# Performance work log

Hardware: AMD Instinct MI355X
Metric: run time of the kernel (lower is better)

## Reference

```python
import jax, jax.numpy as jnp
import numpy as np

B = 1024   # env batch (rollout step, T=1)
F = 512    # feature_size ('big' conv tower)
H = 128    # LSTM hidden size


def _conv(x, W, b, stride):
    # x: [B,Cin,H,W], W: [Cout,Cin,kh,kw]  (PyTorch NCHW / OIHW, VALID padding)
    y = jax.lax.conv_general_dilated(x, W, (stride, stride), 'VALID',
                                     dimension_numbers=('NCHW', 'OIHW', 'NCHW'))
    return y + b[None, :, None, None]


def _tower(x, W1, b1, W2, b2, W3, b3, Wl, bl):
    y = jax.nn.relu(_conv(x, W1, b1, 4))   # [B,32,20,20]
    y = jax.nn.relu(_conv(y, W2, b2, 2))   # [B,64,9,9]
    y = jax.nn.relu(_conv(y, W3, b3, 1))   # [B,64,7,7]
    y = y.reshape(y.shape[0], -1)          # [B,3136]
    return jax.nn.relu(y @ Wl.T + bl)      # [B,512]


def _ln(x, g, b):
    m = jnp.mean(x, -1, keepdims=True)
    v = jnp.var(x, -1, keepdims=True)
    return (x - m) * jax.lax.rsqrt(v + 1e-5) * g + b


def setup_inputs() -> dict:
    key = jax.random.key(0)
    ks = iter(jax.random.split(key, 64))
    rn = lambda shape, s=0.05: jax.random.normal(next(ks), shape, jnp.float32) * s
    inp = {
        'x': jax.random.normal(next(ks), (B, 2, 84, 84), jnp.float32),
        'done': (jax.random.uniform(next(ks), (B,)) < 0.1).astype(jnp.float32),
        'h0': rn((1, B, H), 0.1),
        'c0': rn((1, B, H), 0.1),
        # video tower
        'vW1': rn((32, 1, 8, 8)), 'vb1': jnp.zeros((32,), jnp.float32),
        'vW2': rn((64, 32, 4, 4)), 'vb2': jnp.zeros((64,), jnp.float32),
        'vW3': rn((64, 64, 3, 3)), 'vb3': jnp.zeros((64,), jnp.float32),
        'vWl': rn((F, 64 * 7 * 7)), 'vbl': jnp.zeros((F,), jnp.float32),
        # audio tower
        'aW1': rn((32, 1, 8, 8)), 'ab1': jnp.zeros((32,), jnp.float32),
        'aW2': rn((64, 32, 4, 4)), 'ab2': jnp.zeros((64,), jnp.float32),
        'aW3': rn((64, 64, 3, 3)), 'ab3': jnp.zeros((64,), jnp.float32),
        'aWl': rn((F, 64 * 7 * 7)), 'abl': jnp.zeros((F,), jnp.float32),
        # LayerNorms
        'vln_g': jnp.ones((F,), jnp.float32), 'vln_b': jnp.zeros((F,), jnp.float32),
        'aln_g': jnp.ones((F,), jnp.float32), 'aln_b': jnp.zeros((F,), jnp.float32),
        # CASL attention
        'att_vW': rn((32, F)), 'att_vb': jnp.zeros((32,), jnp.float32),
        'att_aW': rn((32, F)), 'att_ab': jnp.zeros((32,), jnp.float32),
        'att_sW': rn((32, H)), 'att_sb': jnp.zeros((32,), jnp.float32),
        'attW': rn((2, 32)), 'attb': jnp.zeros((2,), jnp.float32),
        # LSTM (PyTorch gate order i,f,g,o)
        'Wih': rn((4 * H, F)), 'Whh': rn((4 * H, H)),
        'bih': jnp.zeros((4 * H,), jnp.float32), 'bhh': jnp.zeros((4 * H,), jnp.float32),
    }
    return inp


def reference(x, done, h0, c0,
              vW1, vb1, vW2, vb2, vW3, vb3, vWl, vbl,
              aW1, ab1, aW2, ab2, aW3, ab3, aWl, abl,
              vln_g, vln_b, aln_g, aln_b,
              att_vW, att_vb, att_aW, att_ab, att_sW, att_sb, attW, attb,
              Wih, Whh, bih, bhh):
    # get_states with T=1 rollout step (batch_size = B)
    vf = _ln(_tower(x[:, 0:1], vW1, vb1, vW2, vb2, vW3, vb3, vWl, vbl), vln_g, vln_b)  # [B,512]
    af = _ln(_tower(x[:, 1:2], aW1, ab1, aW2, ab2, aW3, ab3, aWl, abl), aln_g, aln_b)  # [B,512]
    # attention gating
    act = jnp.tanh(vf @ att_vW.T + att_vb + af @ att_aW.T + att_ab
                   + h0[0] @ att_sW.T + att_sb)                    # [B,32]
    w = jax.nn.softmax(act @ attW.T + attb, axis=-1)               # [B,2]
    fused = w[:, 0:1] * vf + w[:, 1:2] * af                        # [B,512]
    # done-masked LSTM cell (single timestep)
    m = (1.0 - done)[:, None]
    h = m * h0[0]
    c = m * c0[0]
    gates = fused @ Wih.T + bih + h @ Whh.T + bhh                  # [B,512]
    i, f, g, o = jnp.split(gates, 4, axis=-1)
    c_new = jax.nn.sigmoid(f) * c + jax.nn.sigmoid(i) * jnp.tanh(g)
    h_new = jax.nn.sigmoid(o) * jnp.tanh(c_new)                    # [B,128]
    return h_new, c_new, vf, af
```

## Files before the change

kernel.cpp:

```cpp
#include <hip/hip_runtime.h>


typedef unsigned short u16;
typedef unsigned int u32;
typedef __attribute__((ext_vector_type(8))) short bf16x8;
typedef __attribute__((ext_vector_type(4))) float f32x4;

__device__ __forceinline__ float b2f(u16 u) {
    union { u32 i; float f; } v; v.i = ((u32)u) << 16; return v.f;
}
__device__ __forceinline__ u16 f2b(float f) {
    union { float f; u32 i; } v; v.f = f;
    u32 r = v.i + 0x7fffu + ((v.i >> 16) & 1u);
    return (u16)(r >> 16);
}
__device__ __forceinline__ void wave_lds_sync() {
    __builtin_amdgcn_wave_barrier();
    __builtin_amdgcn_s_waitcnt(0xC07F);
    __builtin_amdgcn_wave_barrier();
}

__global__ __launch_bounds__(256) void conv1_mfma(
    const float* __restrict__ x, long boff,
    const u16* __restrict__ Wp,
    const float* __restrict__ bias_v, const float* __restrict__ bias_a,
    u16* __restrict__ outp, int Mtot)
{
    __shared__ __attribute__((aligned(16))) u16 As[4 * 2304];

    const int tid = threadIdx.x;
    const int wave = tid >> 6, lane = tid & 63, quad = lane >> 4, l16 = lane & 15;
    const int t = blockIdx.y;
    const u16* Wpt = Wp + t * 2048;
    const float* bias = t ? bias_a : bias_v;
    u16* outt = outp + (long)t * Mtot * 32;

    const int mbase = blockIdx.x * 128 + wave * 32;
    const int rl = lane >> 1, h = lane & 1;
    int m = mbase + rl; if (m > Mtot - 1) m = Mtot - 1;
    const int bl = m / 400, p = m % 400;
    const int oy = p / 20, ox = p % 20;
    const float* F = x + boff + (long)bl * 14112 + t * 7056
                     + (long)(oy * 4) * 84 + ox * 4;

    {
        u16 tmp[32];
#pragma unroll
        for (int rr = 0; rr < 4; ++rr) {
            const int ky = h * 4 + rr;
            float4 v0 = *(const float4*)(F + ky * 84);
            float4 v1 = *(const float4*)(F + ky * 84 + 4);
            tmp[rr * 8 + 0] = f2b(v0.x); tmp[rr * 8 + 1] = f2b(v0.y);
            tmp[rr * 8 + 2] = f2b(v0.z); tmp[rr * 8 + 3] = f2b(v0.w);
            tmp[rr * 8 + 4] = f2b(v1.x); tmp[rr * 8 + 5] = f2b(v1.y);
            tmp[rr * 8 + 6] = f2b(v1.z); tmp[rr * 8 + 7] = f2b(v1.w);
        }
        u16* dst = As + wave * 2304 + rl * 72 + h * 32;
        const uint4* s = (const uint4*)tmp;
        *(uint4*)(dst)      = s[0];
        *(uint4*)(dst + 8)  = s[1];
        *(uint4*)(dst + 16) = s[2];
        *(uint4*)(dst + 24) = s[3];
    }
    wave_lds_sync();

    const u16* rb = As + wave * 2304;
    f32x4 acc[2][2];
#pragma unroll
    for (int mi = 0; mi < 2; ++mi)
#pragma unroll
        for (int ni = 0; ni < 2; ++ni)
            acc[mi][ni] = (f32x4){0.f, 0.f, 0.f, 0.f};

#pragma unroll
    for (int ks = 0; ks < 2; ++ks) {
        bf16x8 af[2], bf[2];
#pragma unroll
        for (int mi = 0; mi < 2; ++mi)
            af[mi] = *(const bf16x8*)(rb + (mi * 16 + l16) * 72 + ks * 32 + quad * 8);
#pragma unroll
        for (int ni = 0; ni < 2; ++ni)
            bf[ni] = *(const bf16x8*)(Wpt + ((ks * 2 + ni) * 64 + lane) * 8);
#pragma unroll
        for (int mi = 0; mi < 2; ++mi)
#pragma unroll
            for (int ni = 0; ni < 2; ++ni)
                acc[mi][ni] = __builtin_amdgcn_mfma_f32_16x16x32_bf16(
                    af[mi], bf[ni], acc[mi][ni], 0, 0, 0);
    }

#pragma unroll
    for (int mi = 0; mi < 2; ++mi)
#pragma unroll
        for (int ni = 0; ni < 2; ++ni) {
            const int col = ni * 16 + l16;
            const float bv = bias[col];
#pragma unroll
            for (int rr = 0; rr < 4; ++rr) {
                const int row = mbase + mi * 16 + quad * 4 + rr;
                if (row < Mtot)
                    outt[(long)row * 32 + col] = f2b(fmaxf(acc[mi][ni][rr] + bv, 0.f));
            }
        }
}

template<int IC, int IH, int IW, int OC, int KH, int KW, int S, int OH, int OW>
__global__ __launch_bounds__(256) void convW_mfma(
    const u16* __restrict__ in, long inTs,
    const u16* __restrict__ Wp, int WpTs,
    const float* __restrict__ bias_v, const float* __restrict__ bias_a,
    u16* __restrict__ outp, long outTs, int Mtot)
{
    constexpr int OP  = OH * OW;
    constexpr int K   = KH * KW * IC;
    constexpr int NF  = OC / 16;
    constexpr int NCH = K / 64;

    __shared__ __attribute__((aligned(16))) u16 As[4 * 2 * 2304];

    const int tid = threadIdx.x;
    const int wave = tid >> 6, lane = tid & 63, quad = lane >> 4, l16 = lane & 15;
    const int t = blockIdx.y;
    const u16* int_ = in + (long)t * inTs;
    const u16* Wpt = Wp + (long)t * WpTs;
    const float* bias = t ? bias_a : bias_v;
    u16* outt = outp + (long)t * outTs;

    const int mbase = blockIdx.x * 128 + wave * 32;
    const int rl = lane >> 1, h = lane & 1;
    int m = mbase + rl; if (m > Mtot - 1) m = Mtot - 1;
    const int bl = m / OP, p = m % OP;
    const int oy = p / OW, ox = p % OW;
    const u16* abase = int_ + (((long)bl * IH + oy * S) * IW + ox * S) * IC + h * 32;

    u16* wbase = As + wave * 4608 + rl * 72 + h * 32;
    const u16* rbase = As + wave * 4608;

    f32x4 acc[2][NF];
#pragma unroll
    for (int mi = 0; mi < 2; ++mi)
#pragma unroll
        for (int ni = 0; ni < NF; ++ni)
            acc[mi][ni] = (f32x4){0.f, 0.f, 0.f, 0.f};

    uint4 pre0, pre1, pre2, pre3;
    {
        const uint4* s = (const uint4*)abase;
        pre0 = s[0]; pre1 = s[1]; pre2 = s[2]; pre3 = s[3];
    }

#pragma unroll
    for (int c = 0; c < NCH; ++c) {
        {
            u16* dst = wbase + (c & 1) * 2304;
            *(uint4*)(dst)      = pre0;
            *(uint4*)(dst + 8)  = pre1;
            *(uint4*)(dst + 16) = pre2;
            *(uint4*)(dst + 24) = pre3;
        }
        if (c + 1 < NCH) {
            const int k0 = (c + 1) * 64;
            const int pos = k0 / IC;
            const int ky = pos / KW, kx = pos - ky * KW;
            const uint4* s = (const uint4*)(abase + ((long)ky * IW + kx) * IC);
            pre0 = s[0]; pre1 = s[1]; pre2 = s[2]; pre3 = s[3];
        }
        wave_lds_sync();

        const u16* rb = rbase + (c & 1) * 2304;
#pragma unroll
        for (int ks = 0; ks < 2; ++ks) {
            bf16x8 af[2], bf[NF];
#pragma unroll
            for (int mi = 0; mi < 2; ++mi)
                af[mi] = *(const bf16x8*)(rb + (mi * 16 + l16) * 72 + ks * 32 + quad * 8);
#pragma unroll
            for (int ni = 0; ni < NF; ++ni)
                bf[ni] = *(const bf16x8*)(Wpt + (((c * 2 + ks) * NF + ni) * 64 + lane) * 8);
#pragma unroll
            for (int mi = 0; mi < 2; ++mi)
#pragma unroll
                for (int ni = 0; ni < NF; ++ni)
                    acc[mi][ni] = __builtin_amdgcn_mfma_f32_16x16x32_bf16(
                        af[mi], bf[ni], acc[mi][ni], 0, 0, 0);
        }
        __builtin_amdgcn_wave_barrier();
    }

#pragma unroll
    for (int mi = 0; mi < 2; ++mi)
#pragma unroll
        for (int ni = 0; ni < NF; ++ni) {
            const int col = ni * 16 + l16;
            const float bv = bias[col];
#pragma unroll
            for (int rr = 0; rr < 4; ++rr) {
                const int row = mbase + mi * 16 + quad * 4 + rr;
                if (row < Mtot)
                    outt[(long)row * OC + col] = f2b(fmaxf(acc[ni < NF ? mi : mi][ni][rr] + bv, 0.f));
            }
        }
}

#define LDSP 40
__global__ __launch_bounds__(256) void gemm_skp(
    const u16* __restrict__ A, const u16* __restrict__ B0,
    const u16* __restrict__ B1,
    float* __restrict__ Cp, int M, int Mhalf, int N, int K, int Kc)
{
    __shared__ __attribute__((aligned(16))) u16 As[128 * LDSP];
    __shared__ __attribute__((aligned(16))) u16 Bs[128 * LDSP];

    const int tid  = threadIdx.x;
    const int wave = tid >> 6, lane = tid & 63;
    const int quad = lane >> 4, l16 = lane & 15;
    const int m0 = blockIdx.y * 128, n0 = blockIdx.x * 128;
    const u16* B = (m0 < Mhalf) ? B0 : B1;
    const int wm = (wave >> 1) * 64, wn = (wave & 1) * 64;
    const int kfrom = blockIdx.z * Kc;
    int kto = kfrom + Kc; if (kto > K) kto = K;
    float* C = Cp + (long)blockIdx.z * M * N;

    f32x4 acc[4][4];
#pragma unroll
    for (int mi = 0; mi < 4; ++mi)
#pragma unroll
        for (int ni = 0; ni < 4; ++ni)
            acc[mi][ni] = (f32x4){0.f, 0.f, 0.f, 0.f};

    for (int k0 = kfrom; k0 < kto; k0 += 32) {
        __syncthreads();
#pragma unroll
        for (int pass = 0; pass < 2; ++pass) {
            int idx = tid + pass * 256;
            int r = idx >> 2, seg = idx & 3;
            int gr = m0 + r; if (gr > M - 1) gr = M - 1;
            uint4 va = *(const uint4*)(A + (long)gr * K + k0 + seg * 8);
            *(uint4*)(As + r * LDSP + seg * 8) = va;
            uint4 vb = *(const uint4*)(B + (long)(n0 + r) * K + k0 + seg * 8);
            *(uint4*)(Bs + r * LDSP + seg * 8) = vb;
        }
        __syncthreads();

        bf16x8 af[4], bfr[4];
#pragma unroll
        for (int mi = 0; mi < 4; ++mi)
            af[mi] = *(const bf16x8*)(As + (wm + mi * 16 + l16) * LDSP + quad * 8);
#pragma unroll
        for (int ni = 0; ni < 4; ++ni)
            bfr[ni] = *(const bf16x8*)(Bs + (wn + ni * 16 + l16) * LDSP + quad * 8);
#pragma unroll
        for (int mi = 0; mi < 4; ++mi)
#pragma unroll
            for (int ni = 0; ni < 4; ++ni)
                acc[mi][ni] = __builtin_amdgcn_mfma_f32_16x16x32_bf16(
                    af[mi], bfr[ni], acc[mi][ni], 0, 0, 0);
    }

#pragma unroll
    for (int mi = 0; mi < 4; ++mi)
#pragma unroll
        for (int ni = 0; ni < 4; ++ni) {
            int col = n0 + wn + ni * 16 + l16;
#pragma unroll
            for (int rr = 0; rr < 4; ++rr) {
                int row = m0 + wm + mi * 16 + quad * 4 + rr;
                if (row < M) C[(long)row * N + col] = acc[mi][ni][rr];
            }
        }
}

__global__ __launch_bounds__(256) void pack_wl(
    const float* __restrict__ vWl, const float* __restrict__ aWl,
    u16* __restrict__ dst)
{
    __shared__ float row[3136];
    const int bid = blockIdx.x, tid = threadIdx.x;
    const int n = bid & 511;
    const float* src = (bid < 512) ? vWl : aWl;
    for (int i = tid; i < 3136; i += 256)
        row[i] = src[(long)n * 3136 + i];
    __syncthreads();
    u16* d = dst + (long)bid * 3136;
    for (int i = tid; i < 3136; i += 256) {
        int p = i >> 6, oc = i & 63;
        d[i] = f2b(row[oc * 49 + p]);
    }
}

__global__ __launch_bounds__(256) void pack_misc(
    const float* __restrict__ vW1, const float* __restrict__ aW1,
    const float* __restrict__ vW2, const float* __restrict__ aW2,
    const float* __restrict__ vW3, const float* __restrict__ aW3,
    const float* __restrict__ avW, const float* __restrict__ aaW,
    const float* __restrict__ asW,
    const float* __restrict__ Wih, const float* __restrict__ Whh,
    u16* __restrict__ Wp1, u16* __restrict__ Wp2, u16* __restrict__ Wp3,
    u16* __restrict__ WTatt, u16* __restrict__ Bcat)
{
    const int idx = blockIdx.x * 256 + threadIdx.x;
    if (idx < 4096) {
        const float* s = (idx < 2048) ? vW1 : aW1;
        int j0 = idx & 2047;
        int jj = j0 & 7, lane = (j0 >> 3) & 63, rest = j0 >> 9;
        int ni = rest & 1, ks = rest >> 1;
        int oc = ni * 16 + (lane & 15);
        int k  = ks * 32 + (lane >> 4) * 8 + jj;
        Wp1[idx] = f2b(s[oc * 64 + k]);
    } else if (idx < 69632) {
        int i = idx - 4096;
        const float* s = (i < 32768) ? vW2 : aW2;
        int j0 = i & 32767;
        int jj = j0 & 7, lane = (j0 >> 3) & 63, rest = j0 >> 9;
        int ni = rest & 3, rest2 = rest >> 2;
        int ks = rest2 & 1, c = rest2 >> 1;
        int oc = ni * 16 + (lane & 15);
        int k  = c * 64 + ks * 32 + (lane >> 4) * 8 + jj;
        int pos = k >> 5, ic = k & 31;
        int ky = pos >> 2, kx = pos & 3;
        Wp2[i] = f2b(s[((oc * 32 + ic) * 4 + ky) * 4 + kx]);
    } else if (idx < 143360) {
        int i = idx - 69632;
        const float* s = (i < 36864) ? vW3 : aW3;
        int j0 = i % 36864;
        int jj = j0 & 7, lane = (j0 >> 3) & 63, rest = j0 >> 9;
        int ni = rest & 3, rest2 = rest >> 2;
        int ks = rest2 & 1, c = rest2 >> 1;
        int oc = ni * 16 + (lane & 15);
        int k  = c * 64 + ks * 32 + (lane >> 4) * 8 + jj;
        int pos = k >> 6, ic = k & 63;
        int ky = pos / 3, kx = pos % 3;
        Wp3[i] = f2b(s[((oc * 64 + ic) * 3 + ky) * 3 + kx]);
    } else if (idx < 180224) {
        int i = idx - 143360;
        int k = i >> 5, j = i & 31;
        float v = (k < 512) ? avW[(long)j * 512 + k]
                : (k < 1024) ? aaW[(long)j * 512 + (k - 512)]
                : asW[(long)j * 128 + (k - 1024)];
        WTatt[i] = f2b(v);
    } else if (idx < 507904) {
        int i = idx - 180224;
        int n = i / 640, k = i % 640;
        Bcat[i] = f2b((k < 512) ? Wih[(long)n * 512 + k]
                                : Whh[(long)n * 128 + (k - 512)]);
    }
}

__global__ __launch_bounds__(256) void ln_attn(
    const float* __restrict__ ychp,
    const float* __restrict__ bl_v, const float* __restrict__ bl_a,
    const float* __restrict__ g_v,  const float* __restrict__ g_a,
    const float* __restrict__ be_v, const float* __restrict__ be_a,
    const float* __restrict__ h0,   const float* __restrict__ done,
    const u16* __restrict__ WT,
    const float* __restrict__ avb, const float* __restrict__ aab,
    const float* __restrict__ asb,
    const float* __restrict__ attW, const float* __restrict__ attb,
    float* __restrict__ vf_out, float* __restrict__ af_out,
    u16* __restrict__ Acat)
{
    __shared__ float vs[512], afs[512], hs[128], red[256], part[8][32], act[32], wsm[2];
    __shared__ float mean_s, inv_s;
    const int b = blockIdx.x, tid = threadIdx.x;

    if (tid < 128) hs[tid] = h0[b * 128 + tid];

#pragma unroll
    for (int tw = 0; tw < 2; ++tw) {
        const long row = tw ? (1024 + b) : b;
        const float* bias = tw ? bl_a : bl_v;
        const float* g    = tw ? g_a  : g_v;
        const float* be   = tw ? be_a : be_v;
        float* fo   = tw ? af_out : vf_out;
        float* dst  = tw ? afs : vs;

        float s0 = bias[tid], s1 = bias[tid + 256];
#pragma unroll
        for (int z = 0; z < 7; ++z) {
            const float* yr = ychp + (long)z * 1048576 + row * 512;
            s0 += yr[tid];
            s1 += yr[tid + 256];
        }
        float v0 = fmaxf(s0, 0.f), v1 = fmaxf(s1, 0.f);

        __syncthreads();
        red[tid] = v0 + v1;
        __syncthreads();
        for (int s = 128; s > 0; s >>= 1) { if (tid < s) red[tid] += red[tid + s]; __syncthreads(); }
        if (tid == 0) mean_s = red[0] * (1.f / 512.f);
        __syncthreads();
        float mean = mean_s;
        float d0 = v0 - mean, d1 = v1 - mean;
        red[tid] = d0 * d0 + d1 * d1;
        __syncthreads();
        for (int s = 128; s > 0; s >>= 1) { if (tid < s) red[tid] += red[tid + s]; __syncthreads(); }
        if (tid == 0) inv_s = rsqrtf(red[0] * (1.f / 512.f) + 1e-5f);
        __syncthreads();
        float inv = inv_s;

        float o0 = d0 * inv * g[tid]       + be[tid];
        float o1 = d1 * inv * g[tid + 256] + be[tid + 256];
        dst[tid] = o0; dst[tid + 256] = o1;
        fo[(long)b * 512 + tid]       = o0;
        fo[(long)b * 512 + tid + 256] = o1;
    }
    __syncthreads();

    {
        const int j = tid & 31, g = tid >> 5;
        float a = 0.f;
#pragma unroll 8
        for (int k = g * 64; k < g * 64 + 64; ++k)
            a += vs[k] * b2f(WT[k * 32 + j]);
#pragma unroll 8
        for (int k = g * 64; k < g * 64 + 64; ++k)
            a += afs[k] * b2f(WT[(512 + k) * 32 + j]);
#pragma unroll 8
        for (int k = g * 16; k < g * 16 + 16; ++k)
            a += hs[k] * b2f(WT[(1024 + k) * 32 + j]);
        part[g][j] = a;
    }
    __syncthreads();
    if (tid < 32) {
        float a = avb[tid] + aab[tid] + asb[tid];
#pragma unroll
        for (int g2 = 0; g2 < 8; ++g2) a += part[g2][tid];
        act[tid] = tanhf(a);
    }
    __syncthreads();
    if (tid == 0) {
        float l0 = attb[0], l1 = attb[1];
        for (int j = 0; j < 32; ++j) {
            l0 += act[j] * attW[j];
            l1 += act[j] * attW[32 + j];
        }
        float mx = fmaxf(l0, l1);
        float e0 = expf(l0 - mx), e1 = expf(l1 - mx);
        float s = e0 + e1;
        wsm[0] = e0 / s; wsm[1] = e1 / s;
    }
    __syncthreads();
    const float w0 = wsm[0], w1 = wsm[1];
    const float m = 1.f - done[b];
    for (int i = tid; i < 512; i += 256)
        Acat[(long)b * 640 + i] = f2b(w0 * vs[i] + w1 * afs[i]);
    if (tid < 128)
        Acat[(long)b * 640 + 512 + tid] = f2b(m * hs[tid]);
}

__global__ __launch_bounds__(128) void lstm_fin(
    const float* __restrict__ gatesp,
    const float* __restrict__ bih, const float* __restrict__ bhh,
    const float* __restrict__ c0, const float* __restrict__ done,
    float* __restrict__ out)
{
    const int b = blockIdx.x, j = threadIdx.x;
    float gi = bih[j]       + bhh[j];
    float gf = bih[128 + j] + bhh[128 + j];
    float gg = bih[256 + j] + bhh[256 + j];
    float go = bih[384 + j] + bhh[384 + j];
#pragma unroll
    for (int z = 0; z < 4; ++z) {
        const float* G = gatesp + (long)z * 524288 + (long)b * 512;
        gi += G[j]; gf += G[128 + j]; gg += G[256 + j]; go += G[384 + j];
    }
    float m  = 1.f - done[b];
    float c  = m * c0[b * 128 + j];
    float si = 1.f / (1.f + expf(-gi));
    float sf = 1.f / (1.f + expf(-gf));
    float so = 1.f / (1.f + expf(-go));
    float cn = sf * c + si * tanhf(gg);
    float hn = so * tanhf(cn);
    out[b * 128 + j]          = hn;
    out[131072 + b * 128 + j] = cn;
}

extern "C" void kernel_launch(void* const* d_in, const int* in_sizes, int n_in,
                              void* d_out, int out_size, void* d_ws, size_t ws_size,
                              hipStream_t stream)
{
    (void)in_sizes; (void)n_in; (void)out_size;

    const float* x     = (const float*)d_in[0];
    const float* done  = (const float*)d_in[1];
    const float* h0    = (const float*)d_in[2];
    const float* c0in  = (const float*)d_in[3];
    const float* vW1   = (const float*)d_in[4];
    const float* vb1   = (const float*)d_in[5];
    const float* vW2   = (const float*)d_in[6];
    const float* vb2   = (const float*)d_in[7];
    const float* vW3   = (const float*)d_in[8];
    const float* vb3   = (const float*)d_in[9];
    const float* vWl   = (const float*)d_in[10];
    const float* vbl   = (const float*)d_in[11];
    const float* aW1   = (const float*)d_in[12];
    const float* ab1   = (const float*)d_in[13];
    const float* aW2   = (const float*)d_in[14];
    const float* ab2   = (const float*)d_in[15];
    const float* aW3   = (const float*)d_in[16];
    const float* ab3   = (const float*)d_in[17];
    const float* aWl   = (const float*)d_in[18];
    const float* abl   = (const float*)d_in[19];
    const float* vln_g = (const float*)d_in[20];
    const float* vln_b = (const float*)d_in[21];
    const float* aln_g = (const float*)d_in[22];
    const float* aln_b = (const float*)d_in[23];
    const float* att_vW = (const float*)d_in[24];
    const float* att_vb = (const float*)d_in[25];
    const float* att_aW = (const float*)d_in[26];
    const float* att_ab = (const float*)d_in[27];
    const float* att_sW = (const float*)d_in[28];
    const float* att_sb = (const float*)d_in[29];
    const float* attW  = (const float*)d_in[30];
    const float* attb  = (const float*)d_in[31];
    const float* Wih   = (const float*)d_in[32];
    const float* Whh   = (const float*)d_in[33];
    const float* bih   = (const float*)d_in[34];
    const float* bhh   = (const float*)d_in[35];

    float* out = (float*)d_out;
    float* vf_out = out + 262144;
    float* af_out = out + 786432;

    const size_t PERBATCH = 2ul * (12800 + 5184) * 2;
    const size_t PERSIST  =
          4ul * 1024 * 512 * 4
        + 7ul * 2048 * 512 * 4
        + 1024ul * 640 * 2
        + 512ul * 640 * 2
        + 2ul * 512 * 3136 * 2
        + 2ul * 2048 * 2
        + 2ul * 32768 * 2
        + 2ul * 36864 * 2
        + 36864ul * 2
        + 2ul * 1024 * 3136 * 2;
    int NB = 64;
    const int cands[4] = {1024, 512, 256, 128};
    for (int i = 0; i < 4; ++i)
        if (PERSIST + (size_t)cands[i] * PERBATCH <= ws_size) { NB = cands[i]; break; }
    const int NC = 1024 / NB;

    char* p = (char*)d_ws;
    float* gatesp = (float*)p; p += 4ul * 1024 * 512 * 4;
    float* ychp   = (float*)p; p += 7ul * 2048 * 512 * 4;
    u16*   Acat   = (u16*)p;   p += 1024ul * 640 * 2;
    u16*   Bcat   = (u16*)p;   p += 512ul * 640 * 2;
    u16*   Wlb    = (u16*)p;   p += 2ul * 512 * 3136 * 2;
    u16*   Wp1    = (u16*)p;   p += 2ul * 2048 * 2;
    u16*   Wp2    = (u16*)p;   p += 2ul * 32768 * 2;
    u16*   Wp3    = (u16*)p;   p += 2ul * 36864 * 2;
    u16*   WTatt  = (u16*)p;   p += 36864ul * 2;
    u16*   c3f    = (u16*)p;   p += 2ul * 1024 * 3136 * 2;
    u16*   c1     = (u16*)p;   p += 2ul * NB * 12800 * 2;
    u16*   c2     = (u16*)p;

    hipLaunchKernelGGL(pack_wl, dim3(1024), dim3(256), 0, stream, vWl, aWl, Wlb);
    hipLaunchKernelGGL(pack_misc, dim3(1984), dim3(256), 0, stream,
        vW1, aW1, vW2, aW2, vW3, aW3, att_vW, att_aW, att_sW, Wih, Whh,
        Wp1, Wp2, Wp3, WTatt, Bcat);

    for (int cch = 0; cch < NC; ++cch) {
        const int b0 = cch * NB;
        const int M1 = NB * 400, M2 = NB * 81, M3 = NB * 49;

        hipLaunchKernelGGL(conv1_mfma, dim3(M1 / 128, 2), dim3(256), 0, stream,
            x, (long)b0 * 14112, Wp1, vb1, ab1, c1, M1);

        hipLaunchKernelGGL((convW_mfma<32, 20, 20, 64, 4, 4, 2, 9, 9>),
            dim3((M2 + 127) / 128, 2), dim3(256), 0, stream,
            c1, (long)NB * 12800, Wp2, 32768, vb2, ab2,
            c2, (long)NB * 5184, M2);

        hipLaunchKernelGGL((convW_mfma<64, 9, 9, 64, 3, 3, 1, 7, 7>),
            dim3((M3 + 127) / 128, 2), dim3(256), 0, stream,
            c2, (long)NB * 5184, Wp3, 36864, vb3, ab3,
            c3f + (long)b0 * 3136, 1024l * 3136, M3);
    }

    hipLaunchKernelGGL(gemm_skp, dim3(4, 16, 7), dim3(256), 0, stream,
        c3f, Wlb, Wlb + 512ul * 3136, ychp, 2048, 1024, 512, 3136, 448);

    hipLaunchKernelGGL(ln_attn, dim3(1024), dim3(256), 0, stream,
        ychp, vbl, abl, vln_g, aln_g, vln_b, aln_b, h0, done, WTatt,
        att_vb, att_ab, att_sb, attW, attb, vf_out, af_out, Acat);

    hipLaunchKernelGGL(gemm_skp, dim3(4, 8, 4), dim3(256), 0, stream,
        Acat, Bcat, Bcat, gatesp, 1024, 1 << 30, 512, 640, 160);

    hipLaunchKernelGGL(lstm_fin, dim3(1024), dim3(128), 0, stream,
        gatesp, bih, bhh, c0in, done, out);
}
```

Baseline: 301.9 us.

## Replace linear-layer GEMM with fragment-packed weight GEMM and fold weight packing

Adds a new GEMM kernel for the conv-to-linear layer. It reads B weights directly from global memory in a pre-swizzled MFMA fragment layout, and stages only A through per-wave double-buffered LDS with wave-level syncs, so block-wide barriers go away. The fc weight packing moves into the pack_misc kernel, which writes the fragment layout and saves one launch. The trade-off is more register pressure, from 16 accumulator tiles per wave, and weight reuse that now depends on the cache instead of LDS.

```diff
diff --git a/kernel.cpp b/kernel.cpp
--- a/kernel.cpp
+++ b/kernel.cpp
@@ -197,7 +197,90 @@
             for (int rr = 0; rr < 4; ++rr) {
                 const int row = mbase + mi * 16 + quad * 4 + rr;
                 if (row < Mtot)
-                    outt[(long)row * OC + col] = f2b(fmaxf(acc[ni < NF ? mi : mi][ni][rr] + bv, 0.f));
+                    outt[(long)row * OC + col] = f2b(fmaxf(acc[mi][ni][rr] + bv, 0.f));
+            }
+        }
+}
+
+__global__ __launch_bounds__(256) void gemm_wv(
+    const u16* __restrict__ A, const u16* __restrict__ Bf,
+    float* __restrict__ Cp)
+{
+    __shared__ __attribute__((aligned(16))) u16 As[4 * 2 * 2304];
+
+    const int tid = threadIdx.x;
+    const int wave = tid >> 6, lane = tid & 63, quad = lane >> 4, l16 = lane & 15;
+    const int x = blockIdx.x, y = blockIdx.y, z = blockIdx.z;
+    const int t = (y < 8) ? 0 : 1;
+    const u16* Bt = Bf + (long)t * 1605632;
+
+    const int mbase = y * 128 + wave * 32;
+    const int rl = lane >> 1, h = lane & 1;
+    const u16* abase = A + (long)(mbase + rl) * 3136 + h * 32;
+
+    u16* wbase = As + wave * 4608 + rl * 72 + h * 32;
+    const u16* rbase = As + wave * 4608;
+
+    f32x4 acc[2][8];
+#pragma unroll
+    for (int mi = 0; mi < 2; ++mi)
+#pragma unroll
+        for (int ni = 0; ni < 8; ++ni)
+            acc[mi][ni] = (f32x4){0.f, 0.f, 0.f, 0.f};
+
+    const int c0 = z * 7;
+    uint4 pre0, pre1, pre2, pre3;
+    {
+        const uint4* s = (const uint4*)(abase + c0 * 64);
+        pre0 = s[0]; pre1 = s[1]; pre2 = s[2]; pre3 = s[3];
+    }
+
+#pragma unroll
+    for (int cc = 0; cc < 7; ++cc) {
+        {
+            u16* dst = wbase + (cc & 1) * 2304;
+            *(uint4*)(dst)      = pre0;
+            *(uint4*)(dst + 8)  = pre1;
+            *(uint4*)(dst + 16) = pre2;
+            *(uint4*)(dst + 24) = pre3;
+        }
+        if (cc + 1 < 7) {
+            const uint4* s = (const uint4*)(abase + (c0 + cc + 1) * 64);
+            pre0 = s[0]; pre1 = s[1]; pre2 = s[2]; pre3 = s[3];
+        }
+        wave_lds_sync();
+
+        const u16* rb = rbase + (cc & 1) * 2304;
+#pragma unroll
+        for (int ks = 0; ks < 2; ++ks) {
+            bf16x8 af[2], bf[8];
+#pragma unroll
+            for (int mi = 0; mi < 2; ++mi)
+                af[mi] = *(const bf16x8*)(rb + (mi * 16 + l16) * 72 + ks * 32 + quad * 8);
+#pragma unroll
+            for (int ni = 0; ni < 8; ++ni)
+                bf[ni] = *(const bf16x8*)(Bt
+                    + ((((long)x * 49 + (c0 + cc)) * 2 + ks) * 8 + ni) * 512 + lane * 8);
+#pragma unroll
+            for (int mi = 0; mi < 2; ++mi)
+#pragma unroll
+                for (int ni = 0; ni < 8; ++ni)
+                    acc[mi][ni] = __builtin_amdgcn_mfma_f32_16x16x32_bf16(
+                        af[mi], bf[ni], acc[mi][ni], 0, 0, 0);
+        }
+        __builtin_amdgcn_wave_barrier();
+    }
+
+    float* C = Cp + (long)z * 2048 * 512;
+#pragma unroll
+    for (int mi = 0; mi < 2; ++mi)
+#pragma unroll
+        for (int ni = 0; ni < 8; ++ni) {
+            const int col = x * 128 + ni * 16 + l16;
+#pragma unroll
+            for (int rr = 0; rr < 4; ++rr) {
+                const int row = mbase + mi * 16 + quad * 4 + rr;
+                C[(long)row * 512 + col] = acc[mi][ni][rr];
             }
         }
 }
@@ -270,24 +353,6 @@
         }
 }
 
-__global__ __launch_bounds__(256) void pack_wl(
-    const float* __restrict__ vWl, const float* __restrict__ aWl,
-    u16* __restrict__ dst)
-{
-    __shared__ float row[3136];
-    const int bid = blockIdx.x, tid = threadIdx.x;
-    const int n = bid & 511;
-    const float* src = (bid < 512) ? vWl : aWl;
-    for (int i = tid; i < 3136; i += 256)
-        row[i] = src[(long)n * 3136 + i];
-    __syncthreads();
-    u16* d = dst + (long)bid * 3136;
-    for (int i = tid; i < 3136; i += 256) {
-        int p = i >> 6, oc = i & 63;
-        d[i] = f2b(row[oc * 49 + p]);
-    }
-}
-
 __global__ __launch_bounds__(256) void pack_misc(
     const float* __restrict__ vW1, const float* __restrict__ aW1,
     const float* __restrict__ vW2, const float* __restrict__ aW2,
@@ -295,10 +360,34 @@
     const float* __restrict__ avW, const float* __restrict__ aaW,
     const float* __restrict__ asW,
     const float* __restrict__ Wih, const float* __restrict__ Whh,
+    const float* __restrict__ vWl, const float* __restrict__ aWl,
     u16* __restrict__ Wp1, u16* __restrict__ Wp2, u16* __restrict__ Wp3,
-    u16* __restrict__ WTatt, u16* __restrict__ Bcat)
-{
-    const int idx = blockIdx.x * 256 + threadIdx.x;
+    u16* __restrict__ WTatt, u16* __restrict__ Bcat,
+    u16* __restrict__ Wlbf)
+{
+    __shared__ float row[3136];
+    const int tid = threadIdx.x;
+
+    if (blockIdx.x >= 1984) {
+        const int bid = blockIdx.x - 1984;
+        const int t = bid >> 9, n = bid & 511;
+        const float* src = t ? aWl : vWl;
+        for (int i = tid; i < 3136; i += 256)
+            row[i] = src[(long)n * 3136 + i];
+        __syncthreads();
+        const int xx = n >> 7, ni = (n >> 4) & 7, lp = n & 15;
+        u16* dstb = Wlbf + (long)t * 1605632;
+        for (int i = tid; i < 3136; i += 256) {
+            int c = i >> 6, rem = i & 63;
+            int ks = rem >> 5, hi = (rem >> 3) & 3, jj = rem & 7;
+            int lane = hi * 16 + lp;
+            long dst = ((((long)xx * 49 + c) * 2 + ks) * 8 + ni) * 512 + lane * 8 + jj;
+            dstb[dst] = f2b(row[(i & 63) * 49 + (i >> 6)]);
+        }
+        return;
+    }
+
+    const int idx = blockIdx.x * 256 + tid;
     if (idx < 4096) {
         const float* s = (idx < 2048) ? vW1 : aW1;
         int j0 = idx & 2047;
@@ -545,7 +634,7 @@
     float* ychp   = (float*)p; p += 7ul * 2048 * 512 * 4;
     u16*   Acat   = (u16*)p;   p += 1024ul * 640 * 2;
     u16*   Bcat   = (u16*)p;   p += 512ul * 640 * 2;
-    u16*   Wlb    = (u16*)p;   p += 2ul * 512 * 3136 * 2;
+    u16*   Wlbf   = (u16*)p;   p += 2ul * 512 * 3136 * 2;
     u16*   Wp1    = (u16*)p;   p += 2ul * 2048 * 2;
     u16*   Wp2    = (u16*)p;   p += 2ul * 32768 * 2;
     u16*   Wp3    = (u16*)p;   p += 2ul * 36864 * 2;
@@ -554,10 +643,9 @@
     u16*   c1     = (u16*)p;   p += 2ul * NB * 12800 * 2;
     u16*   c2     = (u16*)p;
 
-    hipLaunchKernelGGL(pack_wl, dim3(1024), dim3(256), 0, stream, vWl, aWl, Wlb);
-    hipLaunchKernelGGL(pack_misc, dim3(1984), dim3(256), 0, stream,
+    hipLaunchKernelGGL(pack_misc, dim3(3008), dim3(256), 0, stream,
         vW1, aW1, vW2, aW2, vW3, aW3, att_vW, att_aW, att_sW, Wih, Whh,
-        Wp1, Wp2, Wp3, WTatt, Bcat);
+        vWl, aWl, Wp1, Wp2, Wp3, WTatt, Bcat, Wlbf);
 
     for (int cch = 0; cch < NC; ++cch) {
         const int b0 = cch * NB;
@@ -577,8 +665,8 @@
             c3f + (long)b0 * 3136, 1024l * 3136, M3);
     }
 
-    hipLaunchKernelGGL(gemm_skp, dim3(4, 16, 7), dim3(256), 0, stream,
-        c3f, Wlb, Wlb + 512ul * 3136, ychp, 2048, 1024, 512, 3136, 448);
+    hipLaunchKernelGGL(gemm_wv, dim3(4, 16, 7), dim3(256), 0, stream,
+        c3f, Wlbf, ychp);
 
     hipLaunchKernelGGL(ln_attn, dim3(1024), dim3(256), 0, stream,
         ychp, vbl, abl, vln_g, aln_g, vln_b, aln_b, h0, done, WTatt,
```

New measurement: 302.3 us. No clear change (+0.1%).
